# Performance work log

Hardware: AMD Instinct MI355X
Metric: run time of the kernel (lower is better)

Reference implementation:

```python
import jax, jax.numpy as jnp
import numpy as np

N = 102400   # total nodes (64 graphs x 1600 nodes)
G = 64       # graphs in batch
NPG = N // G
E = 1638400  # total edges (avg degree 16)
EPG = E // G


def _segmean(x, ids, num):
    s = jax.ops.segment_sum(x, ids, num_segments=num)
    c = jax.ops.segment_sum(jnp.ones((x.shape[0], 1), x.dtype), ids, num_segments=num)
    return s / jnp.maximum(c, 1.0)


def setup_inputs() -> dict:
    key = jax.random.key(0)
    ks = jax.random.split(key, 32)
    node_features = jax.random.normal(ks[0], (N, 60), jnp.float32)
    edge_features = jax.random.normal(ks[1], (E, 1), jnp.float32)
    node_graph = jnp.arange(N, dtype=jnp.int32) // NPG
    edge_graph = jnp.arange(E, dtype=jnp.int32) // EPG
    senders = edge_graph * NPG + jax.random.randint(ks[2], (E,), 0, NPG)
    receivers = edge_graph * NPG + jax.random.randint(ks[3], (E,), 0, NPG)

    def W(k, o, i):
        return (jax.random.normal(k, (o, i), jnp.float32) / np.sqrt(i)).astype(jnp.float32)

    def b(k, o):
        return (jax.random.uniform(k, (o,), jnp.float32) * 0.02 - 0.01).astype(jnp.float32)

    p = dict(
        node_features=node_features, edge_features=edge_features,
        senders=senders, receivers=receivers,
        node_graph=node_graph, edge_graph=edge_graph,
        # encoder: EdgeLinear(8, edge=1, sender=60)
        enc_Wee=W(ks[4], 8, 1), enc_Wes=W(ks[5], 8, 60), enc_be=b(ks[6], 8),
        # encoder: NodeLinear(16, incoming=8, node=60)
        enc_Wnn=W(ks[7], 16, 60), enc_Wni=W(ks[8], 16, 8), enc_bn=b(ks[9], 16),
        # encoder: GlobalLinear(4, edge=8, node=16)
        enc_Wge=W(ks[10], 4, 8), enc_Wgn=W(ks[11], 4, 16), enc_bg=b(ks[12], 4),
        # hidden: EdgeLinear(8, edge=8, sender=16, global=4)
        hid_Wee=W(ks[13], 8, 8), hid_Wes=W(ks[14], 8, 16), hid_Weg=W(ks[15], 8, 4), hid_be=b(ks[16], 8),
        # hidden: NodeLinear(16, node=16, incoming=8, global=4)
        hid_Wnn=W(ks[17], 16, 16), hid_Wni=W(ks[18], 16, 8), hid_Wng=W(ks[19], 16, 4), hid_bn=b(ks[20], 16),
        # hidden: GlobalLinear(4, edge=8, node=16, global=4)
        hid_Wge=W(ks[21], 4, 8), hid_Wgn=W(ks[22], 4, 16), hid_Wgg=W(ks[23], 4, 4), hid_bg=b(ks[24], 4),
        # readouts
        ro_Wn=W(ks[25], 1, 16), ro_bn=b(ks[26], 1),
        ro_Wg=W(ks[27], 1, 4), ro_bg=b(ks[28], 1),
    )
    return p


def reference(node_features, edge_features, senders, receivers, node_graph, edge_graph,
              enc_Wee, enc_Wes, enc_be, enc_Wnn, enc_Wni, enc_bn, enc_Wge, enc_Wgn, enc_bg,
              hid_Wee, hid_Wes, hid_Weg, hid_be, hid_Wnn, hid_Wni, hid_Wng, hid_bn,
              hid_Wge, hid_Wgn, hid_Wgg, hid_bg, ro_Wn, ro_bn, ro_Wg, ro_bg):
    hops = 1
    # ---- encoder GN block ----
    e = jax.nn.relu(edge_features @ enc_Wee.T + node_features[senders] @ enc_Wes.T + enc_be)  # [E,8]
    n = jax.nn.relu(node_features @ enc_Wnn.T + _segmean(e, receivers, N) @ enc_Wni.T + enc_bn)  # [N,16]
    g = jax.nn.relu(_segmean(e, edge_graph, G) @ enc_Wge.T + _segmean(n, node_graph, G) @ enc_Wgn.T + enc_bg)  # [G,4]
    # ---- hidden GN blocks (shared weights across hops) ----
    for _ in range(hops):
        e = jax.nn.relu(e @ hid_Wee.T + n[senders] @ hid_Wes.T + g[edge_graph] @ hid_Weg.T + hid_be)
        n = jax.nn.relu(n @ hid_Wnn.T + _segmean(e, receivers, N) @ hid_Wni.T + g[node_graph] @ hid_Wng.T + hid_bn)
        g = jax.nn.relu(_segmean(e, edge_graph, G) @ hid_Wge.T + _segmean(n, node_graph, G) @ hid_Wgn.T + g @ hid_Wgg.T + hid_bg)
    # ---- readouts ----
    nodes_out = jax.nn.sigmoid(n @ ro_Wn.T + ro_bn)    # [N,1]
    globals_out = jax.nn.sigmoid(g @ ro_Wg.T + ro_bg)  # [G,1]
    return nodes_out, globals_out
```

## Files before the change

kernel.cpp:

```cpp
#include <hip/hip_runtime.h>
#include <hip/hip_bf16.h>
#include <hip/hip_fp16.h>

#define NN   102400
#define NG   64
#define NPG  1600
#define NE   1638400
#define EPG  25600
#define EPC  (EPG / 4)

typedef unsigned int u32;
typedef unsigned short u16;

#define OFF_EDAT  0
#define OFF_SPROJ (NE)
#define OFF_PNN   (NE + 8 * NN)
#define OFF_DEG   (NE + 16 * NN)
#define OFF_START (NE + 17 * NN)
#define OFF_H4C   (NE + 18 * NN)
#define OFF_GS    (NE + 22 * NN)
#define GS_ESUM1 0
#define GS_NSUM1 512
#define GS_ESUM2 1536
#define GS_NSUM2 2048
#define GS_G1    3072
#define GS_GPE   3328
#define GS_GPN   3840

struct H8 { __half2 a, b, c, d; };
struct H4 { __half2 a, b; };

__device__ __forceinline__ void unpack8(const H8 v, float* o) {
    float2 t0 = __half22float2(v.a), t1 = __half22float2(v.b);
    float2 t2 = __half22float2(v.c), t3 = __half22float2(v.d);
    o[0]=t0.x; o[1]=t0.y; o[2]=t1.x; o[3]=t1.y; o[4]=t2.x; o[5]=t2.y; o[6]=t3.x; o[7]=t3.y;
}
__device__ __forceinline__ H8 pack8(const float* v) {
    H8 r;
    r.a = __floats2half2_rn(v[0], v[1]); r.b = __floats2half2_rn(v[2], v[3]);
    r.c = __floats2half2_rn(v[4], v[5]); r.d = __floats2half2_rn(v[6], v[7]);
    return r;
}
__device__ __forceinline__ H4 pack4(const float* v) {
    H4 r;
    r.a = __floats2half2_rn(v[0], v[1]); r.b = __floats2half2_rn(v[2], v[3]);
    return r;
}
__device__ __forceinline__ u16 f2bf(float f) {
    u32 u = __float_as_uint(f);
    return (u16)((u + 0x7fffu + ((u >> 16) & 1u)) >> 16);
}
__device__ __forceinline__ float wsum_par(float v) {
#pragma unroll
    for (int o = 2; o <= 32; o <<= 1) v += __shfl_xor(v, o);
    return v;
}
__device__ __forceinline__ float sigmoidf_(float x) { return 1.f / (1.f + expf(-x)); }

__global__ __launch_bounds__(512) void k_hist4(const int* __restrict__ rcv, int* __restrict__ h4) {
    __shared__ int h[NPG];
    const int g = blockIdx.x >> 2, c = blockIdx.x & 3;
    for (int i = threadIdx.x; i < NPG; i += 512) h[i] = 0;
    __syncthreads();
    const int base = g * EPG + c * EPC;
    for (int t = threadIdx.x; t < EPC; t += 512) atomicAdd(&h[rcv[base + t] - g * NPG], 1);
    __syncthreads();
    int* out = h4 + (size_t)(g * 4 + c) * NPG;
    for (int i = threadIdx.x; i < NPG; i += 512) out[i] = h[i];
}

__global__ __launch_bounds__(320) void k_scan(
    int* __restrict__ h4c, int* __restrict__ deg, int* __restrict__ start)
{
    __shared__ int part[320];
    const int g = blockIdx.x, tid = threadIdx.x;
    const int vb = tid * 5;
    int hc[5][4], d[5], pre[5];
    int ts = 0;
#pragma unroll
    for (int i = 0; i < 5; ++i) {
        const int v = vb + i;
#pragma unroll
        for (int c = 0; c < 4; ++c) hc[i][c] = h4c[(size_t)(g * 4 + c) * NPG + v];
        d[i] = hc[i][0] + hc[i][1] + hc[i][2] + hc[i][3];
        pre[i] = ts;
        ts += d[i];
    }
    part[tid] = ts;
    __syncthreads();
    for (int o = 1; o < 320; o <<= 1) {
        const int v = (tid >= o) ? part[tid - o] : 0;
        __syncthreads();
        part[tid] += v;
        __syncthreads();
    }
    const int off = g * EPG + part[tid] - ts;
#pragma unroll
    for (int i = 0; i < 5; ++i) {
        const int v = vb + i;
        const int st = off + pre[i];
        deg[g * NPG + v] = d[i];
        start[g * NPG + v] = st;
        int run = st;
#pragma unroll
        for (int c = 0; c < 4; ++c) {
            h4c[(size_t)(g * 4 + c) * NPG + v] = run;
            run += hc[i][c];
        }
    }
}

__global__ __launch_bounds__(512) void k_scatter4(
    const float* __restrict__ ef, const int* __restrict__ snd, const int* __restrict__ rcv,
    const int* __restrict__ h4c, u32* __restrict__ edat)
{
    __shared__ int cur[NPG];
    const int g = blockIdx.x >> 2, c = blockIdx.x & 3;
    const int* cb = h4c + (size_t)(g * 4 + c) * NPG;
    for (int i = threadIdx.x; i < NPG; i += 512) cur[i] = cb[i];
    __syncthreads();
    const int base = g * EPG + c * EPC;
    for (int t = threadIdx.x; t < EPC; t += 512) {
        const int e = base + t;
        const int r = rcv[e] - g * NPG;
        const int p = atomicAdd(&cur[r], 1);
        const u32 s = (u32)(snd[e] - g * NPG);
        edat[p] = (s << 16) | (u32)f2bf(ef[e]);
    }
}

__global__ __launch_bounds__(256) void k_node_pre(
    const float* __restrict__ nf,
    const float* __restrict__ Wes,
    const float* __restrict__ Wnn,
    const float* __restrict__ ebe, const float* __restrict__ ebn,
    __half* __restrict__ sproj, __half* __restrict__ pnn, float* __restrict__ gs)
{
    __shared__ float wE[480], wN[960];
    for (int i = threadIdx.x; i < 480; i += 256) wE[i] = Wes[i];
    for (int i = threadIdx.x; i < 960; i += 256) wN[i] = Wnn[i];
    if (blockIdx.x == 0) {
        for (int i = threadIdx.x; i < 3072; i += 256) gs[i] = 0.f;
    }
    __syncthreads();
    const int v = blockIdx.x * 256 + threadIdx.x;
    const float4* row = reinterpret_cast<const float4*>(nf + (size_t)v * 60);
    float x[60];
#pragma unroll
    for (int i = 0; i < 15; ++i) {
        const float4 a = row[i];
        x[4 * i] = a.x; x[4 * i + 1] = a.y; x[4 * i + 2] = a.z; x[4 * i + 3] = a.w;
    }
    float pes[8], pn[16];
#pragma unroll
    for (int j = 0; j < 8; ++j) pes[j] = ebe[j];
#pragma unroll
    for (int j = 0; j < 16; ++j) pn[j] = ebn[j];
#pragma unroll
    for (int k = 0; k < 60; ++k) {
        const float xv = x[k];
#pragma unroll
        for (int j = 0; j < 8; ++j)  pes[j] = fmaf(xv, wE[j * 60 + k], pes[j]);
#pragma unroll
        for (int j = 0; j < 16; ++j) pn[j]  = fmaf(xv, wN[j * 60 + k], pn[j]);
    }
    H8* sp = reinterpret_cast<H8*>(sproj) + (size_t)v * 2;
    sp[0] = pack8(pes);
    H8* pp = reinterpret_cast<H8*>(pnn) + (size_t)v * 2;
    pp[0] = pack8(pn); pp[1] = pack8(pn + 8);
}

__global__ __launch_bounds__(256) void k_enc(
    const int* __restrict__ deg, const int* __restrict__ start, const u32* __restrict__ edat,
    __half* __restrict__ sproj, __half* __restrict__ pnn,
    const float* __restrict__ eWee,
    const float* __restrict__ eWni,
    const float* __restrict__ hWes, const float* __restrict__ hWnn,
    float* __restrict__ esum, float* __restrict__ nsum)
{
    __shared__ float wNI[128], wES[128], wNN2[256];
    for (int i = threadIdx.x; i < 128; i += 256) { wNI[i] = eWni[i]; wES[i] = hWes[i]; }
    wNN2[threadIdx.x] = hWnn[threadIdx.x];
    __syncthreads();
    const int t = blockIdx.x * 256 + threadIdx.x;
    const int v = t >> 1, h = t & 1;
    const int g = v / NPG;
    float wee[8];
#pragma unroll
    for (int j = 0; j < 8; ++j) wee[j] = eWee[j];
    const int dg = deg[v];
    const int st = start[v];
    const int half0 = dg >> 1;
    int i = st + (h ? half0 : 0);
    const int iend = st + (h ? dg : half0);
    float m[8];
#pragma unroll
    for (int j = 0; j < 8; ++j) m[j] = 0.f;
    const H8* hb = reinterpret_cast<const H8*>(sproj) + (size_t)g * NPG * 2;

#define ENC_EDGE(W, A) { \
    const float f_ = __uint_as_float(((W) & 0xffffu) << 16); \
    float pv_[8]; unpack8((A), pv_); \
    _Pragma("unroll") \
    for (int j = 0; j < 8; ++j) m[j] += fmaxf(0.f, fmaf(f_, wee[j], pv_[j])); }

    for (; i + 4 <= iend; i += 4) {
        const u32 w0 = edat[i], w1 = edat[i + 1], w2v = edat[i + 2], w3v = edat[i + 3];
        const H8 A0 = hb[(size_t)(w0 >> 16) * 2];
        const H8 A1 = hb[(size_t)(w1 >> 16) * 2];
        const H8 A2 = hb[(size_t)(w2v >> 16) * 2];
        const H8 A3 = hb[(size_t)(w3v >> 16) * 2];
        ENC_EDGE(w0, A0) ENC_EDGE(w1, A1) ENC_EDGE(w2v, A2) ENC_EDGE(w3v, A3)
    }
    for (; i < iend; ++i) {
        const u32 w = edat[i];
        const H8 A = hb[(size_t)(w >> 16) * 2];
        ENC_EDGE(w, A)
    }
#undef ENC_EDGE

#pragma unroll
    for (int j = 0; j < 8; ++j) m[j] += __shfl_xor(m[j], 1);
#pragma unroll
    for (int j = 0; j < 8; ++j) {
        const float s = wsum_par(m[j]);
        if ((threadIdx.x & 63) == 0) atomicAdd(&esum[g * 8 + j], s);
    }
    const float ic = 1.f / fmaxf((float)dg, 1.f);
    float mk[8];
#pragma unroll
    for (int k = 0; k < 8; ++k) mk[k] = m[k] * ic;
    const H8* pp = reinterpret_cast<const H8*>(pnn) + (size_t)v * 2;
    float pn8[8]; unpack8(pp[h], pn8);
    float n1[8];
#pragma unroll
    for (int jj = 0; jj < 8; ++jj) {
        float x = pn8[jj];
#pragma unroll
        for (int k = 0; k < 8; ++k) x = fmaf(mk[k], wNI[(h * 8 + jj) * 8 + k], x);
        n1[jj] = fmaxf(0.f, x);
    }
    float n1o[8];
#pragma unroll
    for (int jj = 0; jj < 8; ++jj) n1o[jj] = __shfl_xor(n1[jj], 1);
    float full[16];
#pragma unroll
    for (int jj = 0; jj < 8; ++jj) {
        full[jj]     = h ? n1o[jj] : n1[jj];
        full[8 + jj] = h ? n1[jj]  : n1o[jj];
    }
    float pe4[4];
#pragma unroll
    for (int oo = 0; oo < 4; ++oo) {
        const int o = h * 4 + oo;
        float x = 0.f;
#pragma unroll
        for (int j = 0; j < 16; ++j) x = fmaf(full[j], wES[o * 16 + j], x);
        pe4[oo] = x;
    }
    *reinterpret_cast<H4*>(sproj + (size_t)v * 16 + 8 + h * 4) = pack4(pe4);
    float pw8[8];
#pragma unroll
    for (int oo = 0; oo < 8; ++oo) {
        const int o = h * 8 + oo;
        float x = 0.f;
#pragma unroll
        for (int j = 0; j < 16; ++j) x = fmaf(full[j], wNN2[o * 16 + j], x);
        pw8[oo] = x;
    }
    reinterpret_cast<H8*>(pnn)[(size_t)v * 2 + h] = pack8(pw8);
#pragma unroll
    for (int jj = 0; jj < 8; ++jj) {
        const float s = wsum_par(n1[jj]);
        if ((threadIdx.x & 63) == h) atomicAdd(&nsum[g * 16 + h * 8 + jj], s);
    }
}

__global__ void k_glob_enc(
    const float* __restrict__ esum1, const float* __restrict__ nsum1,
    const float* __restrict__ Wge, const float* __restrict__ Wgn, const float* __restrict__ bg,
    const float* __restrict__ hWeg, const float* __restrict__ hWng,
    float* __restrict__ g1, float* __restrict__ gpe, float* __restrict__ gpn)
{
    const int g = threadIdx.x;
    if (g >= NG) return;
    float gv[4];
#pragma unroll
    for (int o = 0; o < 4; ++o) {
        float x = bg[o];
#pragma unroll
        for (int k = 0; k < 8; ++k)  x = fmaf(esum1[g * 8 + k] * (1.f / EPG), Wge[o * 8 + k], x);
#pragma unroll
        for (int k = 0; k < 16; ++k) x = fmaf(nsum1[g * 16 + k] * (1.f / NPG), Wgn[o * 16 + k], x);
        gv[o] = fmaxf(0.f, x);
        g1[g * 4 + o] = gv[o];
    }
#pragma unroll
    for (int j = 0; j < 8; ++j) {
        float x = 0.f;
#pragma unroll
        for (int o = 0; o < 4; ++o) x = fmaf(gv[o], hWeg[j * 4 + o], x);
        gpe[g * 8 + j] = x;
    }
#pragma unroll
    for (int j = 0; j < 16; ++j) {
        float x = 0.f;
#pragma unroll
        for (int o = 0; o < 4; ++o) x = fmaf(gv[o], hWng[j * 4 + o], x);
        gpn[g * 16 + j] = x;
    }
}

__global__ __launch_bounds__(256) void k_hid(
    const int* __restrict__ deg, const int* __restrict__ start, const u32* __restrict__ edat,
    const __half* __restrict__ sproj, const __half* __restrict__ pnn,
    const float* __restrict__ eWee,
    const float* __restrict__ hWee, const float* __restrict__ hbe, const float* __restrict__ gpe,
    const float* __restrict__ hWni, const float* __restrict__ hbn, const float* __restrict__ gpn,
    const float* __restrict__ roWn, const float* __restrict__ robn,
    float* __restrict__ esum, float* __restrict__ nsum, float* __restrict__ outn)
{
    __shared__ float w2[64], wNI[128], rW[16];
    for (int i = threadIdx.x; i < 128; i += 256) wNI[i] = hWni[i];
    if (threadIdx.x < 64) w2[threadIdx.x] = hWee[threadIdx.x];
    if (threadIdx.x < 16) rW[threadIdx.x] = roWn[threadIdx.x];
    __syncthreads();
    const int t = blockIdx.x * 256 + threadIdx.x;
    const int v = t >> 1, h = t & 1;
    const int g = v / NPG;
    float wee[8], add2[8];
#pragma unroll
    for (int j = 0; j < 8; ++j) { wee[j] = eWee[j]; add2[j] = gpe[g * 8 + j] + hbe[j]; }
    const int dg = deg[v];
    const int st = start[v];
    const int half0 = dg >> 1;
    int i = st + (h ? half0 : 0);
    const int iend = st + (h ? dg : half0);
    float m2[8];
#pragma unroll
    for (int j = 0; j < 8; ++j) m2[j] = 0.f;
    const H8* hb = reinterpret_cast<const H8*>(sproj) + (size_t)g * NPG * 2;

#define HID_EDGE(W, A, B) { \
    const float f_ = __uint_as_float(((W) & 0xffffu) << 16); \
    float pv_[8], qv_[8]; unpack8((A), pv_); unpack8((B), qv_); \
    float e1_[8]; \
    _Pragma("unroll") \
    for (int j = 0; j < 8; ++j) e1_[j] = fmaxf(0.f, fmaf(f_, wee[j], pv_[j])); \
    _Pragma("unroll") \
    for (int j = 0; j < 8; ++j) { \
        float x_ = qv_[j] + add2[j]; \
        _Pragma("unroll") \
        for (int k = 0; k < 8; ++k) x_ = fmaf(e1_[k], w2[j * 8 + k], x_); \
        m2[j] += fmaxf(0.f, x_); } }

    for (; i + 4 <= iend; i += 4) {
        const u32 w0 = edat[i], w1 = edat[i + 1], w2v = edat[i + 2], w3v = edat[i + 3];
        const size_t s0 = (size_t)(w0 >> 16) * 2, s1 = (size_t)(w1 >> 16) * 2;
        const size_t s2 = (size_t)(w2v >> 16) * 2, s3 = (size_t)(w3v >> 16) * 2;
        const H8 A0 = hb[s0], B0 = hb[s0 + 1];
        const H8 A1 = hb[s1], B1 = hb[s1 + 1];
        const H8 A2 = hb[s2], B2 = hb[s2 + 1];
        const H8 A3 = hb[s3], B3 = hb[s3 + 1];
        HID_EDGE(w0, A0, B0) HID_EDGE(w1, A1, B1) HID_EDGE(w2v, A2, B2) HID_EDGE(w3v, A3, B3)
    }
    for (; i < iend; ++i) {
        const u32 w = edat[i];
        const size_t s = (size_t)(w >> 16) * 2;
        const H8 A = hb[s], B = hb[s + 1];
        HID_EDGE(w, A, B)
    }
#undef HID_EDGE

#pragma unroll
    for (int j = 0; j < 8; ++j) m2[j] += __shfl_xor(m2[j], 1);
#pragma unroll
    for (int j = 0; j < 8; ++j) {
        const float s = wsum_par(m2[j]);
        if ((threadIdx.x & 63) == 0) atomicAdd(&esum[g * 8 + j], s);
    }
    const float ic = 1.f / fmaxf((float)dg, 1.f);
    float mk[8];
#pragma unroll
    for (int k = 0; k < 8; ++k) mk[k] = m2[k] * ic;
    const H8* pp = reinterpret_cast<const H8*>(pnn) + (size_t)v * 2;
    float pn8[8]; unpack8(pp[h], pn8);
    float zp = 0.f;
    float n2[8];
#pragma unroll
    for (int jj = 0; jj < 8; ++jj) {
        const int j = h * 8 + jj;
        float x = pn8[jj] + gpn[g * 16 + j] + hbn[j];
#pragma unroll
        for (int k = 0; k < 8; ++k) x = fmaf(mk[k], wNI[j * 8 + k], x);
        n2[jj] = fmaxf(0.f, x);
        zp = fmaf(n2[jj], rW[j], zp);
    }
    const float z = zp + __shfl_xor(zp, 1);
    if (h == 0) outn[v] = sigmoidf_(z + robn[0]);
#pragma unroll
    for (int jj = 0; jj < 8; ++jj) {
        const float s = wsum_par(n2[jj]);
        if ((threadIdx.x & 63) == h) atomicAdd(&nsum[g * 16 + h * 8 + jj], s);
    }
}

__global__ void k_glob_hid(
    const float* __restrict__ esum2, const float* __restrict__ nsum2, const float* __restrict__ g1,
    const float* __restrict__ hWge, const float* __restrict__ hWgn,
    const float* __restrict__ hWgg, const float* __restrict__ hbg,
    const float* __restrict__ roWg, const float* __restrict__ robg,
    float* __restrict__ outg)
{
    const int g = threadIdx.x;
    if (g >= NG) return;
    float gv[4];
#pragma unroll
    for (int o = 0; o < 4; ++o) {
        float x = hbg[o];
#pragma unroll
        for (int k = 0; k < 8; ++k)  x = fmaf(esum2[g * 8 + k] * (1.f / EPG), hWge[o * 8 + k], x);
#pragma unroll
        for (int k = 0; k < 16; ++k) x = fmaf(nsum2[g * 16 + k] * (1.f / NPG), hWgn[o * 16 + k], x);
#pragma unroll
        for (int k = 0; k < 4; ++k)  x = fmaf(g1[g * 4 + k], hWgg[o * 4 + k], x);
        gv[o] = fmaxf(0.f, x);
    }
    float z = robg[0];
#pragma unroll
    for (int o = 0; o < 4; ++o) z = fmaf(gv[o], roWg[o], z);
    outg[g] = sigmoidf_(z);
}

extern "C" void kernel_launch(void* const* d_in, const int* in_sizes, int n_in,
                              void* d_out, int out_size, void* d_ws, size_t ws_size,
                              hipStream_t stream)
{
    const float* nf   = (const float*)d_in[0];
    const float* ef   = (const float*)d_in[1];
    const int*   snd  = (const int*)d_in[2];
    const int*   rcv  = (const int*)d_in[3];
    const float* eWee = (const float*)d_in[6];
    const float* eWes = (const float*)d_in[7];
    const float* ebe  = (const float*)d_in[8];
    const float* eWnn = (const float*)d_in[9];
    const float* eWni = (const float*)d_in[10];
    const float* ebn  = (const float*)d_in[11];
    const float* eWge = (const float*)d_in[12];
    const float* eWgn = (const float*)d_in[13];
    const float* ebg  = (const float*)d_in[14];
    const float* hWee = (const float*)d_in[15];
    const float* hWes = (const float*)d_in[16];
    const float* hWeg = (const float*)d_in[17];
    const float* hbe  = (const float*)d_in[18];
    const float* hWnn = (const float*)d_in[19];
    const float* hWni = (const float*)d_in[20];
    const float* hWng = (const float*)d_in[21];
    const float* hbn  = (const float*)d_in[22];
    const float* hWge = (const float*)d_in[23];
    const float* hWgn = (const float*)d_in[24];
    const float* hWgg = (const float*)d_in[25];
    const float* hbg  = (const float*)d_in[26];
    const float* roWn = (const float*)d_in[27];
    const float* robn = (const float*)d_in[28];
    const float* roWg = (const float*)d_in[29];
    const float* robg = (const float*)d_in[30];

    float*  ws    = (float*)d_ws;
    u32*    edat  = (u32*)(ws + OFF_EDAT);
    __half* sproj = (__half*)(ws + OFF_SPROJ);
    __half* pnn   = (__half*)(ws + OFF_PNN);
    int*    deg   = (int*)(ws + OFF_DEG);
    int*    start = (int*)(ws + OFF_START);
    int*    h4c   = (int*)(ws + OFF_H4C);
    float*  gs    = ws + OFF_GS;
    float* esum1 = gs + GS_ESUM1;
    float* nsum1 = gs + GS_NSUM1;
    float* esum2 = gs + GS_ESUM2;
    float* nsum2 = gs + GS_NSUM2;
    float* g1    = gs + GS_G1;
    float* gpe   = gs + GS_GPE;
    float* gpn   = gs + GS_GPN;
    float* out   = (float*)d_out;

    k_hist4<<<NG * 4, 512, 0, stream>>>(rcv, h4c);
    k_scan<<<NG, 320, 0, stream>>>(h4c, deg, start);
    k_scatter4<<<NG * 4, 512, 0, stream>>>(ef, snd, rcv, h4c, edat);
    k_node_pre<<<NN / 256, 256, 0, stream>>>(nf, eWes, eWnn, ebe, ebn, sproj, pnn, gs);
    k_enc<<<NN * 2 / 256, 256, 0, stream>>>(deg, start, edat, sproj, pnn,
                                            eWee, eWni, hWes, hWnn, esum1, nsum1);
    k_glob_enc<<<1, 64, 0, stream>>>(esum1, nsum1, eWge, eWgn, ebg, hWeg, hWng, g1, gpe, gpn);
    k_hid<<<NN * 2 / 256, 256, 0, stream>>>(deg, start, edat, sproj, pnn,
                                            eWee, hWee, hbe, gpe, hWni, hbn, gpn,
                                            roWn, robn, esum2, nsum2, out);
    k_glob_hid<<<1, 64, 0, stream>>>(esum2, nsum2, g1, hWge, hWgn, hWgg, hbg, roWg, robg, out + NN);
}
```

Measured before the change: 144.0 us.

## Add sender-sorted edge path with receiver-slot scatter of edge values

Adds a second execution path, used when the workspace is large enough, that builds both receiver and sender CSR orderings. Edge values are computed per sender node, which loads each sender projection once, and are written as fp16 into receiver-sorted slots. A separate per-receiver pass then reduces them contiguously, replacing the random gather of sender features in the receiver loop. It adds extra histogram, scan and scatter kernels, plus a round trip of an E×8 fp16 buffer through memory for each of the two blocks.

Measured after the change: 194.9 us. +35.3%, slower.

```diff
diff --git a/kernel.cpp b/kernel.cpp
--- a/kernel.cpp
+++ b/kernel.cpp
@@ -11,6 +11,463 @@
 
 typedef unsigned int u32;
 typedef unsigned short u16;
+
+struct H8 { __half2 a, b, c, d; };
+struct H4 { __half2 a, b; };
+
+__device__ __forceinline__ void unpack8(const H8 v, float* o) {
+    float2 t0 = __half22float2(v.a), t1 = __half22float2(v.b);
+    float2 t2 = __half22float2(v.c), t3 = __half22float2(v.d);
+    o[0]=t0.x; o[1]=t0.y; o[2]=t1.x; o[3]=t1.y; o[4]=t2.x; o[5]=t2.y; o[6]=t3.x; o[7]=t3.y;
+}
+__device__ __forceinline__ H8 pack8(const float* v) {
+    H8 r;
+    r.a = __floats2half2_rn(v[0], v[1]); r.b = __floats2half2_rn(v[2], v[3]);
+    r.c = __floats2half2_rn(v[4], v[5]); r.d = __floats2half2_rn(v[6], v[7]);
+    return r;
+}
+__device__ __forceinline__ H4 pack4(const float* v) {
+    H4 r;
+    r.a = __floats2half2_rn(v[0], v[1]); r.b = __floats2half2_rn(v[2], v[3]);
+    return r;
+}
+__device__ __forceinline__ u16 f2bf(float f) {
+    u32 u = __float_as_uint(f);
+    return (u16)((u + 0x7fffu + ((u >> 16) & 1u)) >> 16);
+}
+__device__ __forceinline__ float wsum(float v) {
+#pragma unroll
+    for (int o = 32; o >= 1; o >>= 1) v += __shfl_xor(v, o);
+    return v;
+}
+__device__ __forceinline__ float wsum_par(float v) {
+#pragma unroll
+    for (int o = 2; o <= 32; o <<= 1) v += __shfl_xor(v, o);
+    return v;
+}
+__device__ __forceinline__ float sigmoidf_(float x) { return 1.f / (1.f + expf(-x)); }
+
+
+__global__ __launch_bounds__(512) void k_hist4(const int* __restrict__ idx, int* __restrict__ h4) {
+    __shared__ int h[NPG];
+    const int g = blockIdx.x >> 2, c = blockIdx.x & 3;
+    for (int i = threadIdx.x; i < NPG; i += 512) h[i] = 0;
+    __syncthreads();
+    const int base = g * EPG + c * EPC;
+    for (int t = threadIdx.x; t < EPC; t += 512) atomicAdd(&h[idx[base + t] - g * NPG], 1);
+    __syncthreads();
+    int* out = h4 + (size_t)(g * 4 + c) * NPG;
+    for (int i = threadIdx.x; i < NPG; i += 512) out[i] = h[i];
+}
+
+__global__ __launch_bounds__(320) void k_scan(
+    int* __restrict__ h4c, int* __restrict__ deg, int* __restrict__ start)
+{
+    __shared__ int part[320];
+    const int g = blockIdx.x, tid = threadIdx.x;
+    const int vb = tid * 5;
+    int hc[5][4], d[5], pre[5];
+    int ts = 0;
+#pragma unroll
+    for (int i = 0; i < 5; ++i) {
+        const int v = vb + i;
+#pragma unroll
+        for (int c = 0; c < 4; ++c) hc[i][c] = h4c[(size_t)(g * 4 + c) * NPG + v];
+        d[i] = hc[i][0] + hc[i][1] + hc[i][2] + hc[i][3];
+        pre[i] = ts;
+        ts += d[i];
+    }
+    part[tid] = ts;
+    __syncthreads();
+    for (int o = 1; o < 320; o <<= 1) {
+        const int v = (tid >= o) ? part[tid - o] : 0;
+        __syncthreads();
+        part[tid] += v;
+        __syncthreads();
+    }
+    const int off = g * EPG + part[tid] - ts;
+#pragma unroll
+    for (int i = 0; i < 5; ++i) {
+        const int v = vb + i;
+        const int st = off + pre[i];
+        deg[g * NPG + v] = d[i];
+        start[g * NPG + v] = st;
+        int run = st;
+#pragma unroll
+        for (int c = 0; c < 4; ++c) {
+            h4c[(size_t)(g * 4 + c) * NPG + v] = run;
+            run += hc[i][c];
+        }
+    }
+}
+
+__global__ __launch_bounds__(320) void n_scan_local(
+    int* __restrict__ h4c, int* __restrict__ deg, int* __restrict__ startL)
+{
+    __shared__ int part[320];
+    const int g = blockIdx.x, tid = threadIdx.x;
+    const int vb = tid * 5;
+    int hc[5][4], d[5], pre[5];
+    int ts = 0;
+#pragma unroll
+    for (int i = 0; i < 5; ++i) {
+        const int v = vb + i;
+#pragma unroll
+        for (int c = 0; c < 4; ++c) hc[i][c] = h4c[(size_t)(g * 4 + c) * NPG + v];
+        d[i] = hc[i][0] + hc[i][1] + hc[i][2] + hc[i][3];
+        pre[i] = ts;
+        ts += d[i];
+    }
+    part[tid] = ts;
+    __syncthreads();
+    for (int o = 1; o < 320; o <<= 1) {
+        const int v = (tid >= o) ? part[tid - o] : 0;
+        __syncthreads();
+        part[tid] += v;
+        __syncthreads();
+    }
+    const int off = part[tid] - ts;
+#pragma unroll
+    for (int i = 0; i < 5; ++i) {
+        const int v = vb + i;
+        const int st = off + pre[i];
+        deg[g * NPG + v] = d[i];
+        startL[g * NPG + v] = st;
+        int run = st;
+#pragma unroll
+        for (int c = 0; c < 4; ++c) {
+            h4c[(size_t)(g * 4 + c) * NPG + v] = run;
+            run += hc[i][c];
+        }
+    }
+}
+
+__global__ void k_glob_enc(
+    const float* __restrict__ esum1, const float* __restrict__ nsum1,
+    const float* __restrict__ Wge, const float* __restrict__ Wgn, const float* __restrict__ bg,
+    const float* __restrict__ hWeg, const float* __restrict__ hWng,
+    float* __restrict__ g1, float* __restrict__ gpe, float* __restrict__ gpn)
+{
+    const int g = threadIdx.x;
+    if (g >= NG) return;
+    float gv[4];
+#pragma unroll
+    for (int o = 0; o < 4; ++o) {
+        float x = bg[o];
+#pragma unroll
+        for (int k = 0; k < 8; ++k)  x = fmaf(esum1[g * 8 + k] * (1.f / EPG), Wge[o * 8 + k], x);
+#pragma unroll
+        for (int k = 0; k < 16; ++k) x = fmaf(nsum1[g * 16 + k] * (1.f / NPG), Wgn[o * 16 + k], x);
+        gv[o] = fmaxf(0.f, x);
+        g1[g * 4 + o] = gv[o];
+    }
+#pragma unroll
+    for (int j = 0; j < 8; ++j) {
+        float x = 0.f;
+#pragma unroll
+        for (int o = 0; o < 4; ++o) x = fmaf(gv[o], hWeg[j * 4 + o], x);
+        gpe[g * 8 + j] = x;
+    }
+#pragma unroll
+    for (int j = 0; j < 16; ++j) {
+        float x = 0.f;
+#pragma unroll
+        for (int o = 0; o < 4; ++o) x = fmaf(gv[o], hWng[j * 4 + o], x);
+        gpn[g * 16 + j] = x;
+    }
+}
+
+__global__ void k_glob_hid(
+    const float* __restrict__ esum2, const float* __restrict__ nsum2, const float* __restrict__ g1,
+    const float* __restrict__ hWge, const float* __restrict__ hWgn,
+    const float* __restrict__ hWgg, const float* __restrict__ hbg,
+    const float* __restrict__ roWg, const float* __restrict__ robg,
+    float* __restrict__ outg)
+{
+    const int g = threadIdx.x;
+    if (g >= NG) return;
+    float gv[4];
+#pragma unroll
+    for (int o = 0; o < 4; ++o) {
+        float x = hbg[o];
+#pragma unroll
+        for (int k = 0; k < 8; ++k)  x = fmaf(esum2[g * 8 + k] * (1.f / EPG), hWge[o * 8 + k], x);
+#pragma unroll
+        for (int k = 0; k < 16; ++k) x = fmaf(nsum2[g * 16 + k] * (1.f / NPG), hWgn[o * 16 + k], x);
+#pragma unroll
+        for (int k = 0; k < 4; ++k)  x = fmaf(g1[g * 4 + k], hWgg[o * 4 + k], x);
+        gv[o] = fmaxf(0.f, x);
+    }
+    float z = robg[0];
+#pragma unroll
+    for (int o = 0; o < 4; ++o) z = fmaf(gv[o], roWg[o], z);
+    outg[g] = sigmoidf_(z);
+}
+
+#define P2_EDATS  0
+#define P2_DEGR   (NE)
+#define P2_STARTR (NE + NN)
+#define P2_DEGS   (NE + 2 * NN)
+#define P2_STARTS (NE + 3 * NN)
+#define P2_SPROJA (NE + 4 * NN)
+#define P2_PNN    (NE + 8 * NN)
+#define P2_GS     (NE + 16 * NN)
+#define P2_POOL   (NE + 16 * NN + 4864)
+#define P2_NEED_BYTES ((size_t)(P2_POOL + 4 * NE) * 4)
+
+__global__ __launch_bounds__(512) void n_scat_rpos(
+    const int* __restrict__ rcv, const int* __restrict__ h4c_r, int* __restrict__ rpos)
+{
+    __shared__ int cur[NPG];
+    const int g = blockIdx.x >> 2, c = blockIdx.x & 3;
+    const int* cb = h4c_r + (size_t)(g * 4 + c) * NPG;
+    for (int i = threadIdx.x; i < NPG; i += 512) cur[i] = cb[i];
+    __syncthreads();
+    const int base = g * EPG + c * EPC;
+    for (int t = threadIdx.x; t < EPC; t += 512) {
+        const int e = base + t;
+        const int r = rcv[e] - g * NPG;
+        rpos[e] = atomicAdd(&cur[r], 1);
+    }
+}
+
+__global__ __launch_bounds__(512) void n_scat_s(
+    const float* __restrict__ ef, const int* __restrict__ snd,
+    const int* __restrict__ rpos, const int* __restrict__ h4c_s, u32* __restrict__ edat_s)
+{
+    __shared__ int cur[NPG];
+    const int g = blockIdx.x >> 2, c = blockIdx.x & 3;
+    const int* cb = h4c_s + (size_t)(g * 4 + c) * NPG;
+    for (int i = threadIdx.x; i < NPG; i += 512) cur[i] = cb[i];
+    __syncthreads();
+    const int base = g * EPG + c * EPC;
+    for (int t = threadIdx.x; t < EPC; t += 512) {
+        const int e = base + t;
+        const int s = snd[e] - g * NPG;
+        const int p = atomicAdd(&cur[s], 1);
+        edat_s[p] = ((u32)rpos[e] << 16) | (u32)f2bf(ef[e]);
+    }
+}
+
+__global__ __launch_bounds__(256) void n_node_pre(
+    const float* __restrict__ nf,
+    const float* __restrict__ Wes, const float* __restrict__ Wnn,
+    const float* __restrict__ ebe, const float* __restrict__ ebn,
+    __half* __restrict__ sprojA, __half* __restrict__ pnn, float* __restrict__ gs)
+{
+    __shared__ float wE[480], wN[960];
+    for (int i = threadIdx.x; i < 480; i += 256) wE[i] = Wes[i];
+    for (int i = threadIdx.x; i < 960; i += 256) wN[i] = Wnn[i];
+    if (blockIdx.x == 0) {
+        for (int i = threadIdx.x; i < 3072; i += 256) gs[i] = 0.f;
+    }
+    __syncthreads();
+    const int v = blockIdx.x * 256 + threadIdx.x;
+    const float4* row = reinterpret_cast<const float4*>(nf + (size_t)v * 60);
+    float x[60];
+#pragma unroll
+    for (int i = 0; i < 15; ++i) {
+        const float4 a = row[i];
+        x[4 * i] = a.x; x[4 * i + 1] = a.y; x[4 * i + 2] = a.z; x[4 * i + 3] = a.w;
+    }
+    float pes[8], pn[16];
+#pragma unroll
+    for (int j = 0; j < 8; ++j) pes[j] = ebe[j];
+#pragma unroll
+    for (int j = 0; j < 16; ++j) pn[j] = ebn[j];
+#pragma unroll
+    for (int k = 0; k < 60; ++k) {
+        const float xv = x[k];
+#pragma unroll
+        for (int j = 0; j < 8; ++j)  pes[j] = fmaf(xv, wE[j * 60 + k], pes[j]);
+#pragma unroll
+        for (int j = 0; j < 16; ++j) pn[j]  = fmaf(xv, wN[j * 60 + k], pn[j]);
+    }
+    reinterpret_cast<H8*>(sprojA)[v] = pack8(pes);
+    H8* pp = reinterpret_cast<H8*>(pnn) + (size_t)v * 2;
+    pp[0] = pack8(pn); pp[1] = pack8(pn + 8);
+}
+
+__global__ __launch_bounds__(256) void n_a1(
+    const int* __restrict__ deg_s, const int* __restrict__ start_s,
+    const u32* __restrict__ edat_s, const __half* __restrict__ sprojA,
+    const float* __restrict__ eWee, __half* __restrict__ evals)
+{
+    const int v = blockIdx.x * 256 + threadIdx.x;
+    const int g = v / NPG;
+    float wee[8];
+#pragma unroll
+    for (int j = 0; j < 8; ++j) wee[j] = eWee[j];
+    float ps[8];
+    unpack8(reinterpret_cast<const H8*>(sprojA)[v], ps);
+    const int dg = deg_s[v];
+    const int st = start_s[v];
+    H8* ev = reinterpret_cast<H8*>(evals) + (size_t)g * EPG;
+    for (int i = 0; i < dg; ++i) {
+        const u32 w = edat_s[st + i];
+        const float f = __uint_as_float((w & 0xffffu) << 16);
+        const int rp = (int)(w >> 16);
+        float c[8];
+#pragma unroll
+        for (int j = 0; j < 8; ++j) c[j] = fmaxf(0.f, fmaf(f, wee[j], ps[j]));
+        ev[rp] = pack8(c);
+    }
+}
+
+__global__ __launch_bounds__(256) void n_b1(
+    const int* __restrict__ deg_r, const int* __restrict__ startL_r,
+    const __half* __restrict__ evals, __half* __restrict__ pnn,
+    const float* __restrict__ eWni,
+    float* __restrict__ esum, float* __restrict__ nsum)
+{
+    __shared__ float wNI[128];
+    for (int i = threadIdx.x; i < 128; i += 256) wNI[i] = eWni[i];
+    __syncthreads();
+    const int v = blockIdx.x * 256 + threadIdx.x;
+    const int g = v / NPG;
+    const int dg = deg_r[v];
+    const H8* ev = reinterpret_cast<const H8*>(evals) + (size_t)g * EPG + startL_r[v];
+    float m[8];
+#pragma unroll
+    for (int j = 0; j < 8; ++j) m[j] = 0.f;
+    for (int i = 0; i < dg; ++i) {
+        float t[8]; unpack8(ev[i], t);
+#pragma unroll
+        for (int j = 0; j < 8; ++j) m[j] += t[j];
+    }
+#pragma unroll
+    for (int j = 0; j < 8; ++j) {
+        const float s = wsum(m[j]);
+        if ((threadIdx.x & 63) == 0) atomicAdd(&esum[g * 8 + j], s);
+    }
+    const float ic = 1.f / fmaxf((float)dg, 1.f);
+    float mk[8];
+#pragma unroll
+    for (int k = 0; k < 8; ++k) mk[k] = m[k] * ic;
+    H8* pp = reinterpret_cast<H8*>(pnn) + (size_t)v * 2;
+    float pn[16]; unpack8(pp[0], pn); unpack8(pp[1], pn + 8);
+    float n1[16];
+#pragma unroll
+    for (int j = 0; j < 16; ++j) {
+        float x = pn[j];
+#pragma unroll
+        for (int k = 0; k < 8; ++k) x = fmaf(mk[k], wNI[j * 8 + k], x);
+        n1[j] = fmaxf(0.f, x);
+    }
+    pp[0] = pack8(n1); pp[1] = pack8(n1 + 8);
+#pragma unroll
+    for (int j = 0; j < 16; ++j) {
+        const float s = wsum(n1[j]);
+        if ((threadIdx.x & 63) == 0) atomicAdd(&nsum[g * 16 + j], s);
+    }
+}
+
+__global__ __launch_bounds__(256) void n_a2(
+    const int* __restrict__ deg_s, const int* __restrict__ start_s,
+    const u32* __restrict__ edat_s, const __half* __restrict__ sprojA,
+    const __half* __restrict__ pnn,
+    const float* __restrict__ eWee, const float* __restrict__ hWes,
+    const float* __restrict__ hWee, const float* __restrict__ hbe,
+    const float* __restrict__ gpe, __half* __restrict__ evals)
+{
+    __shared__ float wES[128], w2[64];
+    for (int i = threadIdx.x; i < 128; i += 256) wES[i] = hWes[i];
+    if (threadIdx.x < 64) w2[threadIdx.x] = hWee[threadIdx.x];
+    __syncthreads();
+    const int v = blockIdx.x * 256 + threadIdx.x;
+    const int g = v / NPG;
+    float wee[8];
+#pragma unroll
+    for (int j = 0; j < 8; ++j) wee[j] = eWee[j];
+    float ps[8];
+    unpack8(reinterpret_cast<const H8*>(sprojA)[v], ps);
+    const H8* pp = reinterpret_cast<const H8*>(pnn) + (size_t)v * 2;
+    float n1[16]; unpack8(pp[0], n1); unpack8(pp[1], n1 + 8);
+    float pe[8];
+#pragma unroll
+    for (int o = 0; o < 8; ++o) {
+        float x = gpe[g * 8 + o] + hbe[o];
+#pragma unroll
+        for (int j = 0; j < 16; ++j) x = fmaf(n1[j], wES[o * 16 + j], x);
+        pe[o] = x;
+    }
+    const int dg = deg_s[v];
+    const int st = start_s[v];
+    H8* ev = reinterpret_cast<H8*>(evals) + (size_t)g * EPG;
+    for (int i = 0; i < dg; ++i) {
+        const u32 w = edat_s[st + i];
+        const float f = __uint_as_float((w & 0xffffu) << 16);
+        const int rp = (int)(w >> 16);
+        float e1[8];
+#pragma unroll
+        for (int j = 0; j < 8; ++j) e1[j] = fmaxf(0.f, fmaf(f, wee[j], ps[j]));
+        float c[8];
+#pragma unroll
+        for (int j = 0; j < 8; ++j) {
+            float x = pe[j];
+#pragma unroll
+            for (int k = 0; k < 8; ++k) x = fmaf(e1[k], w2[j * 8 + k], x);
+            c[j] = fmaxf(0.f, x);
+        }
+        ev[rp] = pack8(c);
+    }
+}
+
+__global__ __launch_bounds__(256) void n_b2(
+    const int* __restrict__ deg_r, const int* __restrict__ startL_r,
+    const __half* __restrict__ evals, const __half* __restrict__ pnn,
+    const float* __restrict__ hWnn, const float* __restrict__ hWni,
+    const float* __restrict__ hbn, const float* __restrict__ gpn,
+    const float* __restrict__ roWn, const float* __restrict__ robn,
+    float* __restrict__ esum, float* __restrict__ nsum, float* __restrict__ outn)
+{
+    __shared__ float wNN[256], wNI[128], rW[16];
+    wNN[threadIdx.x] = hWnn[threadIdx.x];
+    for (int i = threadIdx.x; i < 128; i += 256) wNI[i] = hWni[i];
+    if (threadIdx.x < 16) rW[threadIdx.x] = roWn[threadIdx.x];
+    __syncthreads();
+    const int v = blockIdx.x * 256 + threadIdx.x;
+    const int g = v / NPG;
+    const int dg = deg_r[v];
+    const H8* ev = reinterpret_cast<const H8*>(evals) + (size_t)g * EPG + startL_r[v];
+    float m2[8];
+#pragma unroll
+    for (int j = 0; j < 8; ++j) m2[j] = 0.f;
+    for (int i = 0; i < dg; ++i) {
+        float t[8]; unpack8(ev[i], t);
+#pragma unroll
+        for (int j = 0; j < 8; ++j) m2[j] += t[j];
+    }
+#pragma unroll
+    for (int j = 0; j < 8; ++j) {
+        const float s = wsum(m2[j]);
+        if ((threadIdx.x & 63) == 0) atomicAdd(&esum[g * 8 + j], s);
+    }
+    const float ic = 1.f / fmaxf((float)dg, 1.f);
+    float mk[8];
+#pragma unroll
+    for (int k = 0; k < 8; ++k) mk[k] = m2[k] * ic;
+    const H8* pp = reinterpret_cast<const H8*>(pnn) + (size_t)v * 2;
+    float n1[16]; unpack8(pp[0], n1); unpack8(pp[1], n1 + 8);
+    float z = robn[0];
+    float n2[16];
+#pragma unroll
+    for (int j = 0; j < 16; ++j) {
+        float x = gpn[g * 16 + j] + hbn[j];
+#pragma unroll
+        for (int k = 0; k < 16; ++k) x = fmaf(n1[k], wNN[j * 16 + k], x);
+#pragma unroll
+        for (int k = 0; k < 8; ++k)  x = fmaf(mk[k], wNI[j * 8 + k], x);
+        n2[j] = fmaxf(0.f, x);
+        z = fmaf(n2[j], rW[j], z);
+    }
+    outn[v] = sigmoidf_(z);
+#pragma unroll
+    for (int j = 0; j < 16; ++j) {
+        const float s = wsum(n2[j]);
+        if ((threadIdx.x & 63) == 0) atomicAdd(&nsum[g * 16 + j], s);
+    }
+}
 
 #define OFF_EDAT  0
 #define OFF_SPROJ (NE)
@@ -27,89 +484,6 @@
 #define GS_GPE   3328
 #define GS_GPN   3840
 
-struct H8 { __half2 a, b, c, d; };
-struct H4 { __half2 a, b; };
-
-__device__ __forceinline__ void unpack8(const H8 v, float* o) {
-    float2 t0 = __half22float2(v.a), t1 = __half22float2(v.b);
-    float2 t2 = __half22float2(v.c), t3 = __half22float2(v.d);
-    o[0]=t0.x; o[1]=t0.y; o[2]=t1.x; o[3]=t1.y; o[4]=t2.x; o[5]=t2.y; o[6]=t3.x; o[7]=t3.y;
-}
-__device__ __forceinline__ H8 pack8(const float* v) {
-    H8 r;
-    r.a = __floats2half2_rn(v[0], v[1]); r.b = __floats2half2_rn(v[2], v[3]);
-    r.c = __floats2half2_rn(v[4], v[5]); r.d = __floats2half2_rn(v[6], v[7]);
-    return r;
-}
-__device__ __forceinline__ H4 pack4(const float* v) {
-    H4 r;
-    r.a = __floats2half2_rn(v[0], v[1]); r.b = __floats2half2_rn(v[2], v[3]);
-    return r;
-}
-__device__ __forceinline__ u16 f2bf(float f) {
-    u32 u = __float_as_uint(f);
-    return (u16)((u + 0x7fffu + ((u >> 16) & 1u)) >> 16);
-}
-__device__ __forceinline__ float wsum_par(float v) {
-#pragma unroll
-    for (int o = 2; o <= 32; o <<= 1) v += __shfl_xor(v, o);
-    return v;
-}
-__device__ __forceinline__ float sigmoidf_(float x) { return 1.f / (1.f + expf(-x)); }
-
-__global__ __launch_bounds__(512) void k_hist4(const int* __restrict__ rcv, int* __restrict__ h4) {
-    __shared__ int h[NPG];
-    const int g = blockIdx.x >> 2, c = blockIdx.x & 3;
-    for (int i = threadIdx.x; i < NPG; i += 512) h[i] = 0;
-    __syncthreads();
-    const int base = g * EPG + c * EPC;
-    for (int t = threadIdx.x; t < EPC; t += 512) atomicAdd(&h[rcv[base + t] - g * NPG], 1);
-    __syncthreads();
-    int* out = h4 + (size_t)(g * 4 + c) * NPG;
-    for (int i = threadIdx.x; i < NPG; i += 512) out[i] = h[i];
-}
-
-__global__ __launch_bounds__(320) void k_scan(
-    int* __restrict__ h4c, int* __restrict__ deg, int* __restrict__ start)
-{
-    __shared__ int part[320];
-    const int g = blockIdx.x, tid = threadIdx.x;
-    const int vb = tid * 5;
-    int hc[5][4], d[5], pre[5];
-    int ts = 0;
-#pragma unroll
-    for (int i = 0; i < 5; ++i) {
-        const int v = vb + i;
-#pragma unroll
-        for (int c = 0; c < 4; ++c) hc[i][c] = h4c[(size_t)(g * 4 + c) * NPG + v];
-        d[i] = hc[i][0] + hc[i][1] + hc[i][2] + hc[i][3];
-        pre[i] = ts;
-        ts += d[i];
-    }
-    part[tid] = ts;
-    __syncthreads();
-    for (int o = 1; o < 320; o <<= 1) {
-        const int v = (tid >= o) ? part[tid - o] : 0;
-        __syncthreads();
-        part[tid] += v;
-        __syncthreads();
-    }
-    const int off = g * EPG + part[tid] - ts;
-#pragma unroll
-    for (int i = 0; i < 5; ++i) {
-        const int v = vb + i;
-        const int st = off + pre[i];
-        deg[g * NPG + v] = d[i];
-        start[g * NPG + v] = st;
-        int run = st;
-#pragma unroll
-        for (int c = 0; c < 4; ++c) {
-            h4c[(size_t)(g * 4 + c) * NPG + v] = run;
-            run += hc[i][c];
-        }
-    }
-}
-
 __global__ __launch_bounds__(512) void k_scatter4(
     const float* __restrict__ ef, const int* __restrict__ snd, const int* __restrict__ rcv,
     const int* __restrict__ h4c, u32* __restrict__ edat)
@@ -131,8 +505,7 @@
 
 __global__ __launch_bounds__(256) void k_node_pre(
     const float* __restrict__ nf,
-    const float* __restrict__ Wes,
-    const float* __restrict__ Wnn,
+    const float* __restrict__ Wes, const float* __restrict__ Wnn,
     const float* __restrict__ ebe, const float* __restrict__ ebn,
     __half* __restrict__ sproj, __half* __restrict__ pnn, float* __restrict__ gs)
 {
@@ -273,41 +646,6 @@
     for (int jj = 0; jj < 8; ++jj) {
         const float s = wsum_par(n1[jj]);
         if ((threadIdx.x & 63) == h) atomicAdd(&nsum[g * 16 + h * 8 + jj], s);
-    }
-}
-
-__global__ void k_glob_enc(
-    const float* __restrict__ esum1, const float* __restrict__ nsum1,
-    const float* __restrict__ Wge, const float* __restrict__ Wgn, const float* __restrict__ bg,
-    const float* __restrict__ hWeg, const float* __restrict__ hWng,
-    float* __restrict__ g1, float* __restrict__ gpe, float* __restrict__ gpn)
-{
-    const int g = threadIdx.x;
-    if (g >= NG) return;
-    float gv[4];
-#pragma unroll
-    for (int o = 0; o < 4; ++o) {
-        float x = bg[o];
-#pragma unroll
-        for (int k = 0; k < 8; ++k)  x = fmaf(esum1[g * 8 + k] * (1.f / EPG), Wge[o * 8 + k], x);
-#pragma unroll
-        for (int k = 0; k < 16; ++k) x = fmaf(nsum1[g * 16 + k] * (1.f / NPG), Wgn[o * 16 + k], x);
-        gv[o] = fmaxf(0.f, x);
-        g1[g * 4 + o] = gv[o];
-    }
-#pragma unroll
-    for (int j = 0; j < 8; ++j) {
-        float x = 0.f;
-#pragma unroll
-        for (int o = 0; o < 4; ++o) x = fmaf(gv[o], hWeg[j * 4 + o], x);
-        gpe[g * 8 + j] = x;
-    }
-#pragma unroll
-    for (int j = 0; j < 16; ++j) {
-        float x = 0.f;
-#pragma unroll
-        for (int o = 0; o < 4; ++o) x = fmaf(gv[o], hWng[j * 4 + o], x);
-        gpn[g * 16 + j] = x;
     }
 }
 
@@ -405,32 +743,6 @@
     }
 }
 
-__global__ void k_glob_hid(
-    const float* __restrict__ esum2, const float* __restrict__ nsum2, const float* __restrict__ g1,
-    const float* __restrict__ hWge, const float* __restrict__ hWgn,
-    const float* __restrict__ hWgg, const float* __restrict__ hbg,
-    const float* __restrict__ roWg, const float* __restrict__ robg,
-    float* __restrict__ outg)
-{
-    const int g = threadIdx.x;
-    if (g >= NG) return;
-    float gv[4];
-#pragma unroll
-    for (int o = 0; o < 4; ++o) {
-        float x = hbg[o];
-#pragma unroll
-        for (int k = 0; k < 8; ++k)  x = fmaf(esum2[g * 8 + k] * (1.f / EPG), hWge[o * 8 + k], x);
-#pragma unroll
-        for (int k = 0; k < 16; ++k) x = fmaf(nsum2[g * 16 + k] * (1.f / NPG), hWgn[o * 16 + k], x);
-#pragma unroll
-        for (int k = 0; k < 4; ++k)  x = fmaf(g1[g * 4 + k], hWgg[o * 4 + k], x);
-        gv[o] = fmaxf(0.f, x);
-    }
-    float z = robg[0];
-#pragma unroll
-    for (int o = 0; o < 4; ++o) z = fmaf(gv[o], roWg[o], z);
-    outg[g] = sigmoidf_(z);
-}
 
 extern "C" void kernel_launch(void* const* d_in, const int* in_sizes, int n_in,
                               void* d_out, int out_size, void* d_ws, size_t ws_size,
@@ -466,32 +778,71 @@
     const float* roWg = (const float*)d_in[29];
     const float* robg = (const float*)d_in[30];
 
-    float*  ws    = (float*)d_ws;
-    u32*    edat  = (u32*)(ws + OFF_EDAT);
-    __half* sproj = (__half*)(ws + OFF_SPROJ);
-    __half* pnn   = (__half*)(ws + OFF_PNN);
-    int*    deg   = (int*)(ws + OFF_DEG);
-    int*    start = (int*)(ws + OFF_START);
-    int*    h4c   = (int*)(ws + OFF_H4C);
-    float*  gs    = ws + OFF_GS;
-    float* esum1 = gs + GS_ESUM1;
-    float* nsum1 = gs + GS_NSUM1;
-    float* esum2 = gs + GS_ESUM2;
-    float* nsum2 = gs + GS_NSUM2;
-    float* g1    = gs + GS_G1;
-    float* gpe   = gs + GS_GPE;
-    float* gpn   = gs + GS_GPN;
-    float* out   = (float*)d_out;
-
-    k_hist4<<<NG * 4, 512, 0, stream>>>(rcv, h4c);
-    k_scan<<<NG, 320, 0, stream>>>(h4c, deg, start);
-    k_scatter4<<<NG * 4, 512, 0, stream>>>(ef, snd, rcv, h4c, edat);
-    k_node_pre<<<NN / 256, 256, 0, stream>>>(nf, eWes, eWnn, ebe, ebn, sproj, pnn, gs);
-    k_enc<<<NN * 2 / 256, 256, 0, stream>>>(deg, start, edat, sproj, pnn,
-                                            eWee, eWni, hWes, hWnn, esum1, nsum1);
-    k_glob_enc<<<1, 64, 0, stream>>>(esum1, nsum1, eWge, eWgn, ebg, hWeg, hWng, g1, gpe, gpn);
-    k_hid<<<NN * 2 / 256, 256, 0, stream>>>(deg, start, edat, sproj, pnn,
-                                            eWee, hWee, hbe, gpe, hWni, hbn, gpn,
-                                            roWn, robn, esum2, nsum2, out);
-    k_glob_hid<<<1, 64, 0, stream>>>(esum2, nsum2, g1, hWge, hWgn, hWgg, hbg, roWg, robg, out + NN);
-}
+    float* ws  = (float*)d_ws;
+    float* out = (float*)d_out;
+
+    if (ws_size >= P2_NEED_BYTES) {
+        u32*    edat_s  = (u32*)(ws + P2_EDATS);
+        int*    deg_r   = (int*)(ws + P2_DEGR);
+        int*    startLr = (int*)(ws + P2_STARTR);
+        int*    deg_s   = (int*)(ws + P2_DEGS);
+        int*    start_s = (int*)(ws + P2_STARTS);
+        __half* sprojA  = (__half*)(ws + P2_SPROJA);
+        __half* pnn     = (__half*)(ws + P2_PNN);
+        float*  gs      = ws + P2_GS;
+        int*    rpos    = (int*)(ws + P2_POOL);
+        int*    h4c_r   = (int*)(ws + P2_POOL + NE);
+        int*    h4c_s   = (int*)(ws + P2_POOL + NE + 4 * NN);
+        __half* evals   = (__half*)(ws + P2_POOL);
+        float* esum1 = gs + GS_ESUM1;
+        float* nsum1 = gs + GS_NSUM1;
+        float* esum2 = gs + GS_ESUM2;
+        float* nsum2 = gs + GS_NSUM2;
+        float* g1    = gs + GS_G1;
+        float* gpe   = gs + GS_GPE;
+        float* gpn   = gs + GS_GPN;
+
+        k_hist4<<<NG * 4, 512, 0, stream>>>(rcv, h4c_r);
+        n_scan_local<<<NG, 320, 0, stream>>>(h4c_r, deg_r, startLr);
+        n_scat_rpos<<<NG * 4, 512, 0, stream>>>(rcv, h4c_r, rpos);
+        k_hist4<<<NG * 4, 512, 0, stream>>>(snd, h4c_s);
+        k_scan<<<NG, 320, 0, stream>>>(h4c_s, deg_s, start_s);
+        n_scat_s<<<NG * 4, 512, 0, stream>>>(ef, snd, rpos, h4c_s, edat_s);
+        n_node_pre<<<NN / 256, 256, 0, stream>>>(nf, eWes, eWnn, ebe, ebn, sprojA, pnn, gs);
+        n_a1<<<NN / 256, 256, 0, stream>>>(deg_s, start_s, edat_s, sprojA, eWee, evals);
+        n_b1<<<NN / 256, 256, 0, stream>>>(deg_r, startLr, evals, pnn, eWni, esum1, nsum1);
+        k_glob_enc<<<1, 64, 0, stream>>>(esum1, nsum1, eWge, eWgn, ebg, hWeg, hWng, g1, gpe, gpn);
+        n_a2<<<NN / 256, 256, 0, stream>>>(deg_s, start_s, edat_s, sprojA, pnn,
+                                           eWee, hWes, hWee, hbe, gpe, evals);
+        n_b2<<<NN / 256, 256, 0, stream>>>(deg_r, startLr, evals, pnn, hWnn, hWni, hbn, gpn,
+                                           roWn, robn, esum2, nsum2, out);
+        k_glob_hid<<<1, 64, 0, stream>>>(esum2, nsum2, g1, hWge, hWgn, hWgg, hbg, roWg, robg, out + NN);
+    } else {
+        u32*    edat  = (u32*)(ws + OFF_EDAT);
+        __half* sproj = (__half*)(ws + OFF_SPROJ);
+        __half* pnn   = (__half*)(ws + OFF_PNN);
+        int*    deg   = (int*)(ws + OFF_DEG);
+        int*    start = (int*)(ws + OFF_START);
+        int*    h4c   = (int*)(ws + OFF_H4C);
+        float*  gs    = ws + OFF_GS;
+        float* esum1 = gs + GS_ESUM1;
+        float* nsum1 = gs + GS_NSUM1;
+        float* esum2 = gs + GS_ESUM2;
+        float* nsum2 = gs + GS_NSUM2;
+        float* g1    = gs + GS_G1;
+        float* gpe   = gs + GS_GPE;
+        float* gpn   = gs + GS_GPN;
+
+        k_hist4<<<NG * 4, 512, 0, stream>>>(rcv, h4c);
+        k_scan<<<NG, 320, 0, stream>>>(h4c, deg, start);
+        k_scatter4<<<NG * 4, 512, 0, stream>>>(ef, snd, rcv, h4c, edat);
+        k_node_pre<<<NN / 256, 256, 0, stream>>>(nf, eWes, eWnn, ebe, ebn, sproj, pnn, gs);
+        k_enc<<<NN * 2 / 256, 256, 0, stream>>>(deg, start, edat, sproj, pnn,
+                                                eWee, eWni, hWes, hWnn, esum1, nsum1);
+        k_glob_enc<<<1, 64, 0, stream>>>(esum1, nsum1, eWge, eWgn, ebg, hWeg, hWng, g1, gpe, gpn);
+        k_hid<<<NN * 2 / 256, 256, 0, stream>>>(deg, start, edat, sproj, pnn,
+                                                eWee, hWee, hbe, gpe, hWni, hbn, gpn,
+                                                roWn, robn, esum2, nsum2, out);
+        k_glob_hid<<<1, 64, 0, stream>>>(esum2, nsum2, g1, hWge, hWgn, hWgg, hbg, roWg, robg, out + NN);
+    }
+}
```
